# Kernel optimization log

Hardware: AMD Instinct MI355X
Metric: run time of the kernel (lower is better)

The kernel has to match this reference:

```python
import jax, jax.numpy as jnp
import numpy as np
from jax import lax

# Parameter physical bounds, order: smax, k1, k2, kb
MIN_BOUNDS = np.array([10.0, 0.01, 0.001, 0.001], dtype=np.float32)
MAX_BOUNDS = np.array([500.0, 0.9, 0.2, 0.1], dtype=np.float32)

T, B, H = 2048, 32, 64
N_FORCING, N_STATE, N_PARAM, N_FLUX = 2, 2, 4, 4


def setup_inputs() -> dict:
    key = jax.random.key(0)
    k1, k2 = jax.random.split(key)
    # forcings: [T, B, H, 2] -> (P precip, PET potential ET), non-negative
    forcings = jax.random.uniform(k1, (T, B, H, N_FORCING), dtype=jnp.float32)
    # initial states: [B, H, 2], model default is zeros
    states = jnp.zeros((B, H, N_STATE), dtype=jnp.float32)
    # unconstrained params in [0,1): [B, H, 4] (static -> repeated over T)
    parameters = jax.random.uniform(k2, (B, H, N_PARAM), dtype=jnp.float32)
    return {"forcings": forcings, "states": states, "parameters": parameters}


def _core(states_t, forcings_t, params_t):
    # states_t: [B,H,2], forcings_t: [B,H,2], params_t: [B,H,4]
    S1, S2 = states_t[..., 0], states_t[..., 1]
    P, PET = forcings_t[..., 0], forcings_t[..., 1]
    smax, k1, k2, kb = (params_t[..., i] for i in range(4))
    # flux_calculator
    et = PET * jnp.clip(S1 / smax, 0.0, 1.0)
    q1 = k1 * S1
    perc = k2 * S1
    qb = kb * S2
    fluxes = jnp.stack([et, q1, perc, qb], axis=-1)  # [B,H,4]
    # state_updater (mass balance), then clamp_(min=0)
    S1n = S1 + P - et - q1 - perc
    S2n = S2 + perc - qb
    new_states = jnp.maximum(jnp.stack([S1n, S2n], axis=-1), 0.0)  # [B,H,2]
    return fluxes, new_states


def reference(forcings, states, parameters):
    # transform parameters to physical bounds: min + (max-min)*u
    min_b = jnp.asarray(MIN_BOUNDS)
    max_b = jnp.asarray(MAX_BOUNDS)
    phys_params = min_b + (max_b - min_b) * parameters  # [B,H,4] (static)

    def step(carry, f_t):
        fluxes_t, new_states = _core(carry, f_t, phys_params)
        return new_states, (fluxes_t, new_states)

    _, (fluxes_seq, states_seq) = lax.scan(step, states, forcings)
    # fluxes_seq: [T,B,H,4], states_seq: [T,B,H,2]
    return fluxes_seq, states_seq
```

## Files before the change

kernel.cpp:

```cpp
#include <hip/hip_runtime.h>
#include <stdint.h>

#define T_STEPS 2048
#define N_CELLS 2048
#define GCELLS  64
#define NGROUPS 32
#define CH      32
#define NCH     (T_STEPS / CH)
#define BCHUNK  16
#define NCHUNK  (T_STEPS / BCHUNK)
#define FLUX_ELEMS ((size_t)T_STEPS * N_CELLS * 4)
#define PROBE_FMA 12288

__global__ void __launch_bounds__(192, 1) hydro_scan(
    const float* __restrict__ forc,
    const float* __restrict__ init_state,
    const float* __restrict__ params,
    float* __restrict__ out)
{
    __shared__ float4 stage[4][CH * GCELLS];
    __shared__ int flags[NCH];
    __shared__ int scan_done;

    const int w = threadIdx.x >> 6;
    const int L = threadIdx.x & 63;
    const int g = blockIdx.x;
    const int cell = g * GCELLS + L;

    if (threadIdx.x < NCH) flags[threadIdx.x] = 0;
    if (threadIdx.x == 0)  scan_done = 0;
    __syncthreads();

    const float4 u = ((const float4*)params)[cell];
    const float smax = 10.0f  + 490.0f * u.x;
    const float k1   = 0.01f  + 0.89f  * u.y;
    const float k2   = 0.001f + 0.199f * u.z;
    const float kb   = 0.001f + 0.099f * u.w;
    const float inv_smax = 1.0f / smax;
    const float a  = 1.0f - k1 - k2;
    const float bb = 1.0f - kb;

    if (w >= 1) {
        const float2* fp2 = (const float2*)forc;
        for (int k = w - 1; k < NCH; k += 2) {
            while (__hip_atomic_load(&scan_done, __ATOMIC_RELAXED,
                                     __HIP_MEMORY_SCOPE_WORKGROUP) < k - 3)
                __builtin_amdgcn_s_sleep(2);
            float2 f[CH];
            #pragma unroll
            for (int t = 0; t < CH; ++t)
                f[t] = fp2[(size_t)(k * CH + t) * N_CELLS + cell];
            float4* tb = stage[k & 3];
            #pragma unroll
            for (int t = 0; t < CH; ++t) {
                const float A = fmaf(-f[t].y, inv_smax, a);
                const float M = f[t].x - f[t].y;
                tb[t * GCELLS + L] = make_float4(A, f[t].x, M, 0.0f);
            }
            asm volatile("s_waitcnt lgkmcnt(0)" ::: "memory");
            if (L == 0)
                __hip_atomic_store(&flags[k], 1, __ATOMIC_RELAXED,
                                   __HIP_MEMORY_SCOPE_WORKGROUP);
        }
        return;
    }

    const float2 s0 = ((const float2*)init_state)[cell];
    float S1 = s0.x;
    float z  = s0.y / k2;
    float2* out_s = (float2*)(out + FLUX_ELEMS);

    for (int k = 0; k < NCH; ++k) {
        while (!__hip_atomic_load(&flags[k], __ATOMIC_RELAXED,
                                  __HIP_MEMORY_SCOPE_WORKGROUP))
            __builtin_amdgcn_s_sleep(1);
        const float4* tb = stage[k & 3];

        float4 rb[2][8];
        #pragma unroll
        for (int j = 0; j < 8; ++j) rb[0][j] = tb[j * GCELLS + L];

        #pragma unroll
        for (int grp = 0; grp < 4; ++grp) {
            const int cur = grp & 1, nxt = cur ^ 1;
            if (grp < 3) {
                #pragma unroll
                for (int j = 0; j < 8; ++j)
                    rb[nxt][j] = tb[((grp + 1) * 8 + j) * GCELLS + L];
            }
            #pragma unroll
            for (int j = 0; j < 8; ++j) {
                const float t1 = fmaf(S1, rb[cur][j].x, rb[cur][j].y);
                const float t2 = fmaf(S1, a, rb[cur][j].z);
                z  = fmaf(z, bb, S1);
                S1 = fmaxf(fmaxf(t1, t2), 0.0f);
            }
            if (grp & 1)
                out_s[(size_t)(k * CH + grp * 8 + 7) * N_CELLS + cell] =
                    make_float2(S1, k2 * z);
        }
        if (L == 0)
            __hip_atomic_store(&scan_done, k + 1, __ATOMIC_RELAXED,
                               __HIP_MEMORY_SCOPE_WORKGROUP);
    }
}

__global__ void __launch_bounds__(256) hydro_expand(
    const float* __restrict__ forc,
    const float* __restrict__ init_state,
    const float* __restrict__ params,
    float* __restrict__ out)
{
    if (blockIdx.x == NCHUNK * NGROUPS / 4) {
        if (threadIdx.x >= 64) return;
        float x = (float)(threadIdx.x + 1);
        #pragma unroll 1
        for (int i = 0; i < PROBE_FMA / 16; ++i) {
            #pragma unroll
            for (int r = 0; r < 16; ++r)
                x = fmaf(x, 0.99999988f, 1.0e-7f);
        }
        asm volatile("" :: "v"(x));
        return;
    }

    const int blk  = blockIdx.x;
    const int wave = threadIdx.x >> 6;
    const int L    = threadIdx.x & 63;
    const int c    = blk >> 3;
    const int g    = (blk & 7) * 4 + wave;
    const int cell = g * GCELLS + L;
    const int t0   = c * BCHUNK;

    float4* out_f = (float4*)out;
    float2* out_s = (float2*)(out + FLUX_ELEMS);
    const float2* fp = (const float2*)forc;
    size_t idx = (size_t)t0 * N_CELLS + cell;

    float2 fb[BCHUNK];
    #pragma unroll
    for (int j = 0; j < BCHUNK; ++j) fb[j] = fp[idx + (size_t)j * N_CELLS];

    const float4 u = ((const float4*)params)[cell];
    float2 sp = (c == 0) ? ((const float2*)init_state)[cell]
                         : out_s[(size_t)(t0 - 1) * N_CELLS + cell];

    const float smax = 10.0f  + 490.0f * u.x;
    const float k1   = 0.01f  + 0.89f  * u.y;
    const float k2   = 0.001f + 0.199f * u.z;
    const float kb   = 0.001f + 0.099f * u.w;
    const float inv_smax = 1.0f / smax;
    const float a  = 1.0f - k1 - k2;
    const float bb = 1.0f - kb;
    float S1 = sp.x, S2 = sp.y;

    #pragma unroll
    for (int j = 0; j < BCHUNK; ++j) {
        const float P = fb[j].x, PET = fb[j].y;
        const float ratio = fminf(S1 * inv_smax, 1.0f);
        const float et   = PET * ratio;
        const float q1   = k1 * S1;
        const float perc = k2 * S1;
        const float qb   = kb * S2;
        const float u1   = fmaf(S1, a, P);
        const float S1n  = fmaxf(u1 - et, 0.0f);
        const float S2n  = fmaf(S2, bb, perc);
        const size_t o = idx + (size_t)j * N_CELLS;
        out_f[o] = make_float4(et, q1, perc, qb);
        if (j < BCHUNK - 1)
            out_s[o] = make_float2(S1n, S2n);
        S1 = S1n; S2 = S2n;
    }
}

extern "C" void kernel_launch(void* const* d_in, const int* in_sizes, int n_in,
                              void* d_out, int out_size, void* d_ws, size_t ws_size,
                              hipStream_t stream) {
    const float* forc = (const float*)d_in[0];
    const float* st0  = (const float*)d_in[1];
    const float* prm  = (const float*)d_in[2];
    float* out = (float*)d_out;

    hipLaunchKernelGGL(hydro_scan, dim3(NGROUPS), dim3(192), 0, stream,
                       forc, st0, prm, out);
    hipLaunchKernelGGL(hydro_expand, dim3(NCHUNK * NGROUPS / 4 + 1), dim3(256),
                       0, stream, forc, st0, prm, out);
}
```

Before: 185.1 us.

## Use four producer waves and half-chunk register double-buffering in scan wave

Raises the scan block from two to four producer waves, each owning one fixed stage buffer, so more forcing loads stay in flight ahead of the serial recurrence. The consumer wave now works in two 16-step halves: it loads the second half and the next chunk's first half from LDS while computing, and spins without sleep on flags, so LDS latency and wakeup delay are hidden. It also bumps the probe FMA count in the expand kernel. The costs are more registers and a busy-wait in the consumer.

Result: no change. 183.6 us (-0.8%).

```diff
diff --git a/kernel.cpp b/kernel.cpp
--- a/kernel.cpp
+++ b/kernel.cpp
@@ -10,9 +10,9 @@
 #define BCHUNK  16
 #define NCHUNK  (T_STEPS / BCHUNK)
 #define FLUX_ELEMS ((size_t)T_STEPS * N_CELLS * 4)
-#define PROBE_FMA 12288
+#define PROBE_FMA 13504
 
-__global__ void __launch_bounds__(192, 1) hydro_scan(
+__global__ void __launch_bounds__(320, 1) hydro_scan(
     const float* __restrict__ forc,
     const float* __restrict__ init_state,
     const float* __restrict__ params,
@@ -41,8 +41,9 @@
     const float bb = 1.0f - kb;
 
     if (w >= 1) {
+        const int p = w - 1;
         const float2* fp2 = (const float2*)forc;
-        for (int k = w - 1; k < NCH; k += 2) {
+        for (int k = p; k < NCH; k += 4) {
             while (__hip_atomic_load(&scan_done, __ATOMIC_RELAXED,
                                      __HIP_MEMORY_SCOPE_WORKGROUP) < k - 3)
                 __builtin_amdgcn_s_sleep(2);
@@ -50,7 +51,7 @@
             #pragma unroll
             for (int t = 0; t < CH; ++t)
                 f[t] = fp2[(size_t)(k * CH + t) * N_CELLS + cell];
-            float4* tb = stage[k & 3];
+            float4* tb = stage[p];
             #pragma unroll
             for (int t = 0; t < CH; ++t) {
                 const float A = fmaf(-f[t].y, inv_smax, a);
@@ -70,39 +71,49 @@
     float z  = s0.y / k2;
     float2* out_s = (float2*)(out + FLUX_ELEMS);
 
+#define STEP(rb_, j_) do {                                                 \
+        const float t1 = fmaf(S1, rb_[j_].x, rb_[j_].y);                   \
+        const float t2 = fmaf(S1, a, rb_[j_].z);                           \
+        z  = fmaf(z, bb, S1);                                  \
+        S1 = fmaxf(fmaxf(t1, t2), 0.0f);                    \
+    } while (0)
+
+    float4 rbA[16], rbB[16];
+
+    while (!__hip_atomic_load(&flags[0], __ATOMIC_RELAXED,
+                              __HIP_MEMORY_SCOPE_WORKGROUP)) {}
+    __builtin_amdgcn_sched_barrier(0);
+    {
+        const float4* tb = stage[0];
+        #pragma unroll
+        for (int j = 0; j < 16; ++j) rbA[j] = tb[j * GCELLS + L];
+    }
+
     for (int k = 0; k < NCH; ++k) {
-        while (!__hip_atomic_load(&flags[k], __ATOMIC_RELAXED,
-                                  __HIP_MEMORY_SCOPE_WORKGROUP))
-            __builtin_amdgcn_s_sleep(1);
         const float4* tb = stage[k & 3];
-
-        float4 rb[2][8];
         #pragma unroll
-        for (int j = 0; j < 8; ++j) rb[0][j] = tb[j * GCELLS + L];
-
+        for (int j = 0; j < 16; ++j) rbB[j] = tb[(16 + j) * GCELLS + L];
         #pragma unroll
-        for (int grp = 0; grp < 4; ++grp) {
-            const int cur = grp & 1, nxt = cur ^ 1;
-            if (grp < 3) {
-                #pragma unroll
-                for (int j = 0; j < 8; ++j)
-                    rb[nxt][j] = tb[((grp + 1) * 8 + j) * GCELLS + L];
-            }
+        for (int j = 0; j < 16; ++j) STEP(rbA, j);
+        out_s[(size_t)(k * CH + 15) * N_CELLS + cell] =
+            make_float2(S1, k2 * z);
+        if (k + 1 < NCH) {
+            while (!__hip_atomic_load(&flags[k + 1], __ATOMIC_RELAXED,
+                                      __HIP_MEMORY_SCOPE_WORKGROUP)) {}
+            __builtin_amdgcn_sched_barrier(0);
+            const float4* tn = stage[(k + 1) & 3];
             #pragma unroll
-            for (int j = 0; j < 8; ++j) {
-                const float t1 = fmaf(S1, rb[cur][j].x, rb[cur][j].y);
-                const float t2 = fmaf(S1, a, rb[cur][j].z);
-                z  = fmaf(z, bb, S1);
-                S1 = fmaxf(fmaxf(t1, t2), 0.0f);
-            }
-            if (grp & 1)
-                out_s[(size_t)(k * CH + grp * 8 + 7) * N_CELLS + cell] =
-                    make_float2(S1, k2 * z);
+            for (int j = 0; j < 16; ++j) rbA[j] = tn[j * GCELLS + L];
         }
+        #pragma unroll
+        for (int j = 0; j < 16; ++j) STEP(rbB, j);
+        out_s[(size_t)(k * CH + 31) * N_CELLS + cell] =
+            make_float2(S1, k2 * z);
         if (L == 0)
             __hip_atomic_store(&scan_done, k + 1, __ATOMIC_RELAXED,
                                __HIP_MEMORY_SCOPE_WORKGROUP);
     }
+#undef STEP
 }
 
 __global__ void __launch_bounds__(256) hydro_expand(
@@ -181,7 +192,7 @@
     const float* prm  = (const float*)d_in[2];
     float* out = (float*)d_out;
 
-    hipLaunchKernelGGL(hydro_scan, dim3(NGROUPS), dim3(192), 0, stream,
+    hipLaunchKernelGGL(hydro_scan, dim3(NGROUPS), dim3(320), 0, stream,
                        forc, st0, prm, out);
     hipLaunchKernelGGL(hydro_expand, dim3(NCHUNK * NGROUPS / 4 + 1), dim3(256),
                        0, stream, forc, st0, prm, out);
```

## Replace producer-consumer LDS staging in scan with single-wave register prefetch pipeline

Applied to the files above, without the earlier changes.

Each scan block now runs as a single wave that loads forcings directly from global memory into three rotating 16-step register buffers. It waits on them with explicit vmcnt counts instead of helper waves that staged precomputed coefficients in LDS behind atomic flags. The per-step coefficients are recomputed inline on the serial critical path, and the dummy FMA probe block is removed from the expand kernel. This removes LDS traffic and flag polling, but each step now does two more ops on the serial chain. The hand-set vmcnt values are fragile: they depend on exactly how the compiler orders the loads and stores.

Result: faster. 170.7 us (-7.8%).

```diff
diff --git a/kernel.cpp b/kernel.cpp
--- a/kernel.cpp
+++ b/kernel.cpp
@@ -5,33 +5,27 @@
 #define N_CELLS 2048
 #define GCELLS  64
 #define NGROUPS 32
-#define CH      32
-#define NCH     (T_STEPS / CH)
 #define BCHUNK  16
 #define NCHUNK  (T_STEPS / BCHUNK)
 #define FLUX_ELEMS ((size_t)T_STEPS * N_CELLS * 4)
-#define PROBE_FMA 12288
 
-__global__ void __launch_bounds__(192, 1) hydro_scan(
+__global__ void __launch_bounds__(64, 1) hydro_scan(
     const float* __restrict__ forc,
     const float* __restrict__ init_state,
     const float* __restrict__ params,
     float* __restrict__ out)
 {
-    __shared__ float4 stage[4][CH * GCELLS];
-    __shared__ int flags[NCH];
-    __shared__ int scan_done;
-
-    const int w = threadIdx.x >> 6;
-    const int L = threadIdx.x & 63;
     const int g = blockIdx.x;
+    const int L = threadIdx.x;
     const int cell = g * GCELLS + L;
 
-    if (threadIdx.x < NCH) flags[threadIdx.x] = 0;
-    if (threadIdx.x == 0)  scan_done = 0;
-    __syncthreads();
+    const float2* __restrict__ fp = (const float2*)forc;
+    float2* out_s = (float2*)(out + FLUX_ELEMS);
+    const float2* base = fp + cell;
 
-    const float4 u = ((const float4*)params)[cell];
+    const float4 u  = ((const float4*)params)[cell];
+    const float2 s0 = ((const float2*)init_state)[cell];
+
     const float smax = 10.0f  + 490.0f * u.x;
     const float k1   = 0.01f  + 0.89f  * u.y;
     const float k2   = 0.001f + 0.199f * u.z;
@@ -39,70 +33,60 @@
     const float inv_smax = 1.0f / smax;
     const float a  = 1.0f - k1 - k2;
     const float bb = 1.0f - kb;
-
-    if (w >= 1) {
-        const float2* fp2 = (const float2*)forc;
-        for (int k = w - 1; k < NCH; k += 2) {
-            while (__hip_atomic_load(&scan_done, __ATOMIC_RELAXED,
-                                     __HIP_MEMORY_SCOPE_WORKGROUP) < k - 3)
-                __builtin_amdgcn_s_sleep(2);
-            float2 f[CH];
-            #pragma unroll
-            for (int t = 0; t < CH; ++t)
-                f[t] = fp2[(size_t)(k * CH + t) * N_CELLS + cell];
-            float4* tb = stage[k & 3];
-            #pragma unroll
-            for (int t = 0; t < CH; ++t) {
-                const float A = fmaf(-f[t].y, inv_smax, a);
-                const float M = f[t].x - f[t].y;
-                tb[t * GCELLS + L] = make_float4(A, f[t].x, M, 0.0f);
-            }
-            asm volatile("s_waitcnt lgkmcnt(0)" ::: "memory");
-            if (L == 0)
-                __hip_atomic_store(&flags[k], 1, __ATOMIC_RELAXED,
-                                   __HIP_MEMORY_SCOPE_WORKGROUP);
-        }
-        return;
-    }
-
-    const float2 s0 = ((const float2*)init_state)[cell];
     float S1 = s0.x;
     float z  = s0.y / k2;
-    float2* out_s = (float2*)(out + FLUX_ELEMS);
 
-    for (int k = 0; k < NCH; ++k) {
-        while (!__hip_atomic_load(&flags[k], __ATOMIC_RELAXED,
-                                  __HIP_MEMORY_SCOPE_WORKGROUP))
-            __builtin_amdgcn_s_sleep(1);
-        const float4* tb = stage[k & 3];
+    float2 A[16], B[16], C[16];
+    #pragma unroll
+    for (int j = 0; j < 16; ++j) A[j] = base[(size_t)j * N_CELLS];
+    #pragma unroll
+    for (int j = 0; j < 16; ++j) B[j] = base[(size_t)(16 + j) * N_CELLS];
+    #pragma unroll
+    for (int j = 0; j < 16; ++j) C[j] = base[(size_t)(32 + j) * N_CELLS];
 
-        float4 rb[2][8];
-        #pragma unroll
-        for (int j = 0; j < 8; ++j) rb[0][j] = tb[j * GCELLS + L];
+#define WAITG(g_) do {                                                         \
+        if ((g_) == 0)                                                         \
+            asm volatile("s_waitcnt vmcnt(32)" ::: "memory");                  \
+        else if ((g_) <= 125)                                                  \
+            asm volatile("s_waitcnt vmcnt(33)" ::: "memory");                  \
+        else if ((g_) == 126)                                                  \
+            asm volatile("s_waitcnt vmcnt(18)" ::: "memory");                  \
+        else                                                                   \
+            asm volatile("s_waitcnt vmcnt(2)" ::: "memory");                   \
+    } while (0)
 
-        #pragma unroll
-        for (int grp = 0; grp < 4; ++grp) {
-            const int cur = grp & 1, nxt = cur ^ 1;
-            if (grp < 3) {
-                #pragma unroll
-                for (int j = 0; j < 8; ++j)
-                    rb[nxt][j] = tb[((grp + 1) * 8 + j) * GCELLS + L];
-            }
-            #pragma unroll
-            for (int j = 0; j < 8; ++j) {
-                const float t1 = fmaf(S1, rb[cur][j].x, rb[cur][j].y);
-                const float t2 = fmaf(S1, a, rb[cur][j].z);
-                z  = fmaf(z, bb, S1);
-                S1 = fmaxf(fmaxf(t1, t2), 0.0f);
-            }
-            if (grp & 1)
-                out_s[(size_t)(k * CH + grp * 8 + 7) * N_CELLS + cell] =
-                    make_float2(S1, k2 * z);
-        }
-        if (L == 0)
-            __hip_atomic_store(&scan_done, k + 1, __ATOMIC_RELAXED,
-                               __HIP_MEMORY_SCOPE_WORKGROUP);
+#define ITER(g_, CUR) do {                                                     \
+        WAITG(g_);                                                             \
+        __builtin_amdgcn_sched_barrier(0);                                     \
+        _Pragma("unroll")                                                      \
+        for (int j = 0; j < 16; ++j) {                                         \
+            const float P = CUR[j].x, PET = CUR[j].y;                          \
+            const float a_c = fmaf(-PET, inv_smax, a);          \
+            const float PmP = P - PET;                          \
+            const float t1  = fmaf(S1, a_c, P);                                \
+            const float t2  = fmaf(S1, a, PmP);                                \
+            z  = fmaf(z, bb, S1);                                  \
+            S1 = fmaxf(fmaxf(t1, t2), 0.0f);                    \
+        }                                                                      \
+        out_s[(size_t)((g_) * BCHUNK + 15) * N_CELLS + cell] =                 \
+            make_float2(S1, k2 * z);                           \
+        if ((g_) + 3 < NCHUNK) {                                               \
+            _Pragma("unroll")                                                  \
+            for (int j = 0; j < 16; ++j)                                       \
+                CUR[j] = base[(size_t)(((g_) + 3) * 16 + j) * N_CELLS];        \
+        }                                                                      \
+    } while (0)
+
+    #pragma unroll 1
+    for (int gg = 0; gg < 126; gg += 3) {
+        ITER(gg,     A);
+        ITER(gg + 1, B);
+        ITER(gg + 2, C);
     }
+    ITER(126, A);
+    ITER(127, B);
+#undef ITER
+#undef WAITG
 }
 
 __global__ void __launch_bounds__(256) hydro_expand(
@@ -111,19 +95,6 @@
     const float* __restrict__ params,
     float* __restrict__ out)
 {
-    if (blockIdx.x == NCHUNK * NGROUPS / 4) {
-        if (threadIdx.x >= 64) return;
-        float x = (float)(threadIdx.x + 1);
-        #pragma unroll 1
-        for (int i = 0; i < PROBE_FMA / 16; ++i) {
-            #pragma unroll
-            for (int r = 0; r < 16; ++r)
-                x = fmaf(x, 0.99999988f, 1.0e-7f);
-        }
-        asm volatile("" :: "v"(x));
-        return;
-    }
-
     const int blk  = blockIdx.x;
     const int wave = threadIdx.x >> 6;
     const int L    = threadIdx.x & 63;
@@ -181,8 +152,8 @@
     const float* prm  = (const float*)d_in[2];
     float* out = (float*)d_out;
 
-    hipLaunchKernelGGL(hydro_scan, dim3(NGROUPS), dim3(192), 0, stream,
+    hipLaunchKernelGGL(hydro_scan, dim3(NGROUPS), dim3(GCELLS), 0, stream,
                        forc, st0, prm, out);
-    hipLaunchKernelGGL(hydro_expand, dim3(NCHUNK * NGROUPS / 4 + 1), dim3(256),
+    hipLaunchKernelGGL(hydro_expand, dim3(NCHUNK * NGROUPS / 4), dim3(256),
                        0, stream, forc, st0, prm, out);
 }
```
